# Optimization experiments

Hardware: AMD Instinct MI355X
Metric: run time of the kernel (lower is better)

## Reference

```python
import jax, jax.numpy as jnp
import numpy as np

G = 64        # graphs per batch
NPG = 1024    # nodes per graph (static)
DEG = 8       # avg degree
INF = 128
HID = 256
OUT = 256
N = G * NPG
E = N * DEG
K1 = 512      # ceil(0.5 * 1024)
K2 = 256      # ceil(0.5 * 512)
EPS = 1e-5


def setup_inputs() -> dict:
    key = jax.random.key(0)
    ks = jax.random.split(key, 12)
    s = 0.05
    x = jax.random.normal(ks[0], (N, INF), jnp.float32)
    off = (jnp.arange(G, dtype=jnp.int32) * NPG)[:, None]
    src = (jax.random.randint(ks[1], (G, NPG * DEG), 0, NPG, jnp.int32) + off).reshape(-1)
    dst = (jax.random.randint(ks[2], (G, NPG * DEG), 0, NPG, jnp.int32) + off).reshape(-1)
    return {
        'x': x, 'src': src, 'dst': dst,
        'W_rel1': jax.random.normal(ks[3], (INF, HID), jnp.float32) * s,
        'b_rel1': jnp.zeros((HID,), jnp.float32),
        'W_root1': jax.random.normal(ks[4], (INF, HID), jnp.float32) * s,
        'g1': jnp.ones((HID,), jnp.float32), 'bt1': jnp.zeros((HID,), jnp.float32),
        'p1': jax.random.normal(ks[5], (HID,), jnp.float32) * s,
        'g2': jnp.ones((HID,), jnp.float32), 'bt2': jnp.zeros((HID,), jnp.float32),
        'W_rel2': jax.random.normal(ks[6], (HID, HID), jnp.float32) * s,
        'b_rel2': jnp.zeros((HID,), jnp.float32),
        'W_root2': jax.random.normal(ks[7], (HID, HID), jnp.float32) * s,
        'p2': jax.random.normal(ks[8], (HID,), jnp.float32) * s,
        'Wl': jax.random.normal(ks[9], (2 * HID, OUT), jnp.float32) * s,
        'bl': jnp.zeros((OUT,), jnp.float32),
    }


def _bn(x, g, b):
    # training-mode BatchNorm over nodes (biased variance), as nn.BatchNorm1d
    m = x.mean(0)
    v = x.var(0)
    return (x - m) * jax.lax.rsqrt(v + EPS) * g + b


def _conv(x, src, dst, emask, W_rel, b_rel, W_root):
    # GraphConv: sum_{j->i} x_j, then lin_rel(aggr) + lin_root(x)
    msg = x[src]                                    # [E, F] gather
    if emask is not None:
        msg = jnp.where(emask[:, None], msg, 0.0)   # dropped edges contribute 0
    agg = jax.ops.segment_sum(msg, dst, num_segments=x.shape[0])
    return agg @ W_rel + b_rel + x @ W_root


def _pool(x, src, dst, emask, p, n, k):
    # TopKPooling: score = tanh((x.p)/||p||); keep top-k per graph; x *= score
    score = jnp.tanh((x @ p) / jnp.linalg.norm(p))  # [G*n]
    vals, idx = jax.lax.top_k(score.reshape(G, n), k)   # [G, k] per-graph
    perm = (idx + (jnp.arange(G, dtype=jnp.int32) * n)[:, None]).reshape(-1)
    xn = x[perm] * vals.reshape(-1)[:, None]        # [G*k, F]
    # remap old node ids -> new ids; -1 marks dropped nodes
    mapping = jnp.full((G * n,), -1, jnp.int32).at[perm].set(
        jnp.arange(G * k, dtype=jnp.int32))
    ns, nd = mapping[src], mapping[dst]
    nmask = emask & (ns >= 0) & (nd >= 0)
    ns = jnp.where(nmask, ns, 0)
    nd = jnp.where(nmask, nd, 0)
    return xn, ns, nd, nmask


def reference(x, src, dst, W_rel1, b_rel1, W_root1, g1, bt1, p1,
              g2, bt2, W_rel2, b_rel2, W_root2, p2, Wl, bl):
    act = lambda v: jax.nn.gelu(v, approximate=False)
    h = _conv(x, src, dst, None, W_rel1, b_rel1, W_root1)
    h = _bn(act(h), g1, bt1)
    h, s1, d1, m1 = _pool(h, src, dst, jnp.ones((E,), bool), p1, NPG, K1)
    hg = h.reshape(G, K1, HID)
    x1 = jnp.concatenate([hg.max(1), hg.mean(1)], axis=1)   # [G, 2H] gmp|gap
    h = act(_bn(h, g2, bt2))
    h = _conv(h, s1, d1, m1, W_rel2, b_rel2, W_root2)
    h, s2, d2, m2 = _pool(h, s1, d1, m1, p2, K1, K2)
    hg = h.reshape(G, K2, HID)
    x2 = jnp.concatenate([hg.max(1), hg.mean(1)], axis=1)
    return (x1 + x2) @ Wl + bl                              # [G, OUT]
```

## Files before the change

### kernel.cpp

```cpp
#include <hip/hip_runtime.h>
#include <hip/hip_bf16.h>
#include <float.h>

#define GG    64
#define NPG   1024
#define EPG   8192
#define NE    524288
#define FIN   128
#define HID   256
#define K1    512
#define K2    256
#define NN0   65536
#define NN1   32768
#define NN2   16384
#define EPSBN 1e-5f

typedef _Float16 f16x8 __attribute__((ext_vector_type(8)));
typedef _Float16 f16x4 __attribute__((ext_vector_type(4)));
typedef float f32x4 __attribute__((ext_vector_type(4)));

__device__ __forceinline__ float gelu_exact(float v) {
    return 0.5f * v * (1.0f + erff(v * 0.7071067811865476f));
}

__device__ __forceinline__ void gld16(const void* g, void* lds) {
    __builtin_amdgcn_global_load_lds(
        (const __attribute__((address_space(1))) unsigned int*)g,
        (__attribute__((address_space(3))) unsigned int*)lds, 16, 0, 0);
}

__global__ __launch_bounds__(512) void k_prepcsr(
        const int* __restrict__ src, const int* __restrict__ dst,
        int* __restrict__ rowp, int* __restrict__ ssrc, int* __restrict__ map1,
        const float* __restrict__ Wrel1, const float* __restrict__ Wroot1,
        const float* __restrict__ Wrel2, const float* __restrict__ Wroot2,
        const float* __restrict__ p2,
        _Float16* __restrict__ W1h, _Float16* __restrict__ W2h,
        float* __restrict__ q2, float* __restrict__ stats1,
        float* __restrict__ stats2) {
    __shared__ int cnt[NPG];
    __shared__ int sa[NPG];
    __shared__ int sb[NPG];
    __shared__ float red[256];
    const int b = blockIdx.x, tid = threadIdx.x;
    if (b < 64) {
        const int g = b;
        const int eb = g * EPG;
        for (int i = g * 512 + tid; i < NN0; i += GG * 512) map1[i] = -1;
        for (int i = tid; i < NPG; i += 512) cnt[i] = 0;
        __syncthreads();
        for (int e = tid; e < EPG; e += 512)
            atomicAdd(&cnt[dst[eb + e] & (NPG - 1)], 1);
        __syncthreads();
        for (int i = tid; i < NPG; i += 512) sa[i] = cnt[i];
        __syncthreads();
        int* cur = sa; int* nxt = sb;
        for (int d = 1; d < NPG; d <<= 1) {
            for (int i = tid; i < NPG; i += 512)
                nxt[i] = cur[i] + ((i >= d) ? cur[i - d] : 0);
            __syncthreads();
            int* t = cur; cur = nxt; nxt = t;
        }
        for (int i = tid; i < NPG; i += 512) {
            const int st = cur[i] - cnt[i];
            rowp[g * (NPG + 1) + i] = st;
            cnt[i] = st;
        }
        if (tid == 0) rowp[g * (NPG + 1) + NPG] = EPG;
        __syncthreads();
        for (int e = tid; e < EPG; e += 512) {
            const int d = dst[eb + e] & (NPG - 1);
            const int p = atomicAdd(&cnt[d], 1);
            ssrc[eb + p] = src[eb + e] & (NPG - 1);
        }
    } else if (b < 192) {
        const int i = (b - 64) * 512 + tid;
        const int n = i >> 8, k = i & 255;
        const float v = (k < FIN) ? Wrel1[k * HID + n] : Wroot1[(k - FIN) * HID + n];
        W1h[i] = (_Float16)v;
    } else if (b < 448) {
        const int i = (b - 192) * 512 + tid;
        const int n = i >> 9, k = i & 511;
        const float v = (k < HID) ? Wrel2[k * HID + n] : Wroot2[(k - HID) * HID + n];
        W2h[i] = (_Float16)v;
    } else if (b == 448) {
        if (tid < 256) { const float pv = p2[tid]; red[tid] = pv * pv; }
        __syncthreads();
        for (int s = 128; s > 0; s >>= 1) {
            if (tid < s) red[tid] += red[tid + s];
            __syncthreads();
        }
        if (tid < 256) q2[tid] = p2[tid] * rsqrtf(red[0]);
    } else {
        stats1[tid] = 0.f;
        stats2[tid] = 0.f;
    }
}

__global__ __launch_bounds__(256) void k_agg1(const float* __restrict__ x,
        const int* __restrict__ rowp, const int* __restrict__ ssrc,
        _Float16* __restrict__ A1) {
    const int b = blockIdx.x;
    const int g = b & 63;
    const int ng = b >> 6;
    const int tid = threadIdx.x;
    const int ln = tid & 31;
    const int node = (ng << 3) + (tid >> 5);
    const int s0 = rowp[g * (NPG + 1) + node];
    const int s1 = rowp[g * (NPG + 1) + node + 1];
    const float4* x4 = reinterpret_cast<const float4*>(x);
    const size_t gb = (size_t)(g << 10) * 32;
    const int* sp = ssrc + (size_t)g * EPG;
    float4 acc = make_float4(0.f, 0.f, 0.f, 0.f);
    for (int j = s0; j < s1; ++j) {
        const float4 v = x4[gb + (size_t)sp[j] * 32 + ln];
        acc.x += v.x; acc.y += v.y; acc.z += v.z; acc.w += v.w;
    }
    const size_t rb = ((size_t)((g << 10) + node)) * 256;
    *reinterpret_cast<f16x4*>(&A1[rb + (ln << 2)]) =
        (f16x4){(_Float16)acc.x, (_Float16)acc.y, (_Float16)acc.z, (_Float16)acc.w};
    const float4 xv = x4[gb + (size_t)node * 32 + ln];
    *reinterpret_cast<f16x4*>(&A1[rb + 128 + (ln << 2)]) =
        (f16x4){(_Float16)xv.x, (_Float16)xv.y, (_Float16)xv.z, (_Float16)xv.w};
}

__global__ __launch_bounds__(256) void k_agg2(const _Float16* __restrict__ A2r,
        const int* __restrict__ rowp, const int* __restrict__ ssrc,
        const int* __restrict__ perm1, const int* __restrict__ map1,
        _Float16* __restrict__ A2w) {
    const int b = blockIdx.x;
    const int g = b & 63;
    const int ng = b >> 6;
    const int tid = threadIdx.x;
    const int ln = tid & 63;
    const int ni = (ng << 2) + (tid >> 6);
    const int on = perm1[(g << 9) + ni] & (NPG - 1);
    const int s0 = rowp[g * (NPG + 1) + on];
    const int s1 = rowp[g * (NPG + 1) + on + 1];
    const int* sp = ssrc + (size_t)g * EPG;
    const int* mp = map1 + ((size_t)g << 10);
    float4 acc = make_float4(0.f, 0.f, 0.f, 0.f);
    for (int j = s0; j < s1; ++j) {
        const int ms = mp[sp[j]];
        if (ms < 0) continue;
        const f16x4 v = *reinterpret_cast<const f16x4*>(
            &A2r[(size_t)ms * 512 + 256 + (ln << 2)]);
        acc.x += (float)v[0]; acc.y += (float)v[1];
        acc.z += (float)v[2]; acc.w += (float)v[3];
    }
    *reinterpret_cast<f16x4*>(&A2w[((size_t)((g << 9) + ni)) * 512 + (ln << 2)]) =
        (f16x4){(_Float16)acc.x, (_Float16)acc.y, (_Float16)acc.z, (_Float16)acc.w};
}

template<int K, int EPI, int MCH>
__global__ __launch_bounds__(512, 2) void k_gemmB(
        const _Float16* __restrict__ A, const _Float16* __restrict__ B,
        const float* __restrict__ bias, _Float16* __restrict__ C,
        float* __restrict__ stats, const float* __restrict__ qv2,
        float* __restrict__ scores, int M) {
    __shared__ _Float16 Bs[256 * 256];
    __shared__ float csum[256];
    __shared__ float csq[256];
    const int tid = threadIdx.x;
    const int l = tid & 63, w = tid >> 6;
    constexpr int BM = 8 * MCH * 16;
    const int m0 = blockIdx.x * BM;
    const int r16 = l & 15, kg = l >> 4;

    f32x4 acc[MCH][16] = {};
    constexpr int PH = K / 256;

#pragma unroll
    for (int ph = 0; ph < PH; ++ph) {
        if (ph) __syncthreads();
        for (int u = tid; u < 8192; u += 512) {
            const int row = u >> 5, slot = u & 31;
            const int gch = slot ^ (row & 7);
            gld16(B + (size_t)row * K + ph * 256 + gch * 8, (char*)Bs + u * 16);
        }
        asm volatile("s_waitcnt vmcnt(0)" ::: "memory");
        __syncthreads();

#pragma unroll
        for (int ks = 0; ks < 8; ++ks) {
            f16x8 a[MCH];
#pragma unroll
            for (int mc = 0; mc < MCH; ++mc) {
                const int mrow = m0 + (w * MCH + mc) * 16 + r16;
                a[mc] = *reinterpret_cast<const f16x8*>(
                    A + (size_t)mrow * K + ph * 256 + ks * 32 + kg * 8);
            }
#pragma unroll
            for (int ni = 0; ni < 16; ++ni) {
                const int brow = ni * 16 + r16;
                const int c = ks * 4 + kg;
                const int pos = c ^ (brow & 7);
                const f16x8 bf = *reinterpret_cast<const f16x8*>(
                    (const char*)Bs + (brow * 32 + pos) * 16);
#pragma unroll
                for (int mc = 0; mc < MCH; ++mc)
                    acc[mc][ni] = __builtin_amdgcn_mfma_f32_16x16x32_f16(
                        a[mc], bf, acc[mc][ni], 0, 0, 0);
            }
        }
    }

    if (EPI == 1) {
        __syncthreads();
        if (tid < 256) { csum[tid] = 0.f; csq[tid] = 0.f; }
        __syncthreads();
    }

    float sp[MCH][4];
    if (EPI == 2) {
#pragma unroll
        for (int mc = 0; mc < MCH; ++mc)
#pragma unroll
            for (int r = 0; r < 4; ++r) sp[mc][r] = 0.f;
    }
#pragma unroll
    for (int ni = 0; ni < 16; ++ni) {
        const int col = ni * 16 + r16;
        const float bc = bias[col];
        const float qvn = (EPI == 2) ? qv2[col] : 0.f;
        float sA = 0.f, qA = 0.f;
#pragma unroll
        for (int mc = 0; mc < MCH; ++mc) {
#pragma unroll
            for (int r = 0; r < 4; ++r) {
                const int row = m0 + (w * MCH + mc) * 16 + (kg << 2) + r;
                float t = acc[mc][ni][r] + bc;
                if (EPI == 1) {
                    t = gelu_exact(t);
                    sA += t;
                    qA += t * t;
                }
                if (EPI == 2) sp[mc][r] += t * qvn;
                C[(size_t)row * 256 + col] = (_Float16)t;
            }
        }
        if (EPI == 1) {
            unsafeAtomicAdd(&csum[col], sA);
            unsafeAtomicAdd(&csq[col], qA);
        }
    }
    if (EPI == 1) {
        __syncthreads();
        if (tid < 256) {
            unsafeAtomicAdd(&stats[tid], csum[tid]);
            unsafeAtomicAdd(&stats[HID + tid], csq[tid]);
        }
    }
    if (EPI == 2) {
#pragma unroll
        for (int mc = 0; mc < MCH; ++mc)
#pragma unroll
            for (int r = 0; r < 4; ++r) {
                float s = sp[mc][r];
                s += __shfl_xor(s, 1);
                s += __shfl_xor(s, 2);
                s += __shfl_xor(s, 4);
                s += __shfl_xor(s, 8);
                if (r16 == 0)
                    scores[m0 + (w * MCH + mc) * 16 + (kg << 2) + r] = s;
            }
    }
}

__global__ __launch_bounds__(256) void k_finalize1(const float* __restrict__ stats,
        const float* __restrict__ g1, const float* __restrict__ bt1,
        const float* __restrict__ p1, float* __restrict__ scale,
        float* __restrict__ shift, float* __restrict__ q, float* __restrict__ r) {
    __shared__ float red[256];
    const int c = threadIdx.x;
    const float m = stats[c] * (1.f / NN0);
    const float v = stats[HID + c] * (1.f / NN0) - m * m;
    const float sc = g1[c] * rsqrtf(v + EPSBN);
    const float sh = bt1[c] - m * sc;
    scale[c] = sc;
    shift[c] = sh;
    const float pv = p1[c];
    red[c] = pv * pv;
    __syncthreads();
    for (int s = 128; s > 0; s >>= 1) {
        if (c < s) red[c] += red[c + s];
        __syncthreads();
    }
    const float inv = rsqrtf(red[0]);
    q[c] = sc * pv * inv;
    __syncthreads();
    red[c] = sh * pv * inv;
    __syncthreads();
    for (int s = 128; s > 0; s >>= 1) {
        if (c < s) red[c] += red[c + s];
        __syncthreads();
    }
    if (c == 0) r[0] = red[0];
}

__global__ __launch_bounds__(256) void k_finalize2(const float* __restrict__ stats,
        const float* __restrict__ g2, const float* __restrict__ bt2,
        float* __restrict__ scale, float* __restrict__ shift) {
    const int c = threadIdx.x;
    const float m = stats[c] * (1.f / NN1);
    const float v = stats[HID + c] * (1.f / NN1) - m * m;
    const float sc = g2[c] * rsqrtf(v + EPSBN);
    scale[c] = sc;
    shift[c] = bt2[c] - m * sc;
}

__global__ __launch_bounds__(256) void k_score(const _Float16* __restrict__ H,
        const float* __restrict__ q, const float* __restrict__ r,
        float* __restrict__ out) {
    const int node = blockIdx.x * 4 + (threadIdx.x >> 6);
    const int lane = threadIdx.x & 63;
    const f16x4 h = *reinterpret_cast<const f16x4*>(H + (size_t)node * HID + (lane << 2));
    const float4 qv = *reinterpret_cast<const float4*>(q + (lane << 2));
    float d = (float)h[0] * qv.x + (float)h[1] * qv.y +
              (float)h[2] * qv.z + (float)h[3] * qv.w;
#pragma unroll
    for (int off = 32; off > 0; off >>= 1) d += __shfl_xor(d, off);
    if (lane == 0) out[node] = d + (r ? r[0] : 0.f);
}

template<int NN_, int KK_, int NT_>
__global__ __launch_bounds__(NT_) void k_topk(const float* __restrict__ scores,
        int nparts, int pstride, int* __restrict__ perm,
        float* __restrict__ vals, int* __restrict__ mapping) {
    __shared__ float s[NN_];
    __shared__ int id[NN_];
    const int g = blockIdx.x, tid = threadIdx.x;
    for (int i = tid; i < NN_; i += NT_) {
        float raw = 0.f;
        for (int p = 0; p < nparts; ++p)
            raw += scores[(size_t)p * pstride + g * NN_ + i];
        s[i] = tanhf(raw);
        id[i] = i;
    }
    __syncthreads();
    for (int k = 2; k <= NN_; k <<= 1) {
        for (int j = k >> 1; j > 0; j >>= 1) {
            for (int t = tid; t < NN_; t += NT_) {
                const int ixj = t ^ j;
                if (ixj > t) {
                    const bool desc = ((t & k) == 0);
                    const float s1 = s[t], s2 = s[ixj];
                    const int i1 = id[t], i2 = id[ixj];
                    const bool inOrder = (s1 > s2) || (s1 == s2 && i1 < i2);
                    if (inOrder != desc) { s[t] = s2; s[ixj] = s1; id[t] = i2; id[ixj] = i1; }
                }
            }
            __syncthreads();
        }
    }
    for (int i = tid; i < KK_; i += NT_) {
        const int oid = id[i];
        perm[g * KK_ + i] = g * NN_ + oid;
        vals[g * KK_ + i] = s[i];
        if (mapping) mapping[g * NN_ + oid] = g * KK_ + i;
    }
}

__global__ __launch_bounds__(256) void k_pool1p(const _Float16* __restrict__ HG,
        const int* __restrict__ perm, const float* __restrict__ vals,
        const float* __restrict__ scale1, const float* __restrict__ shift1,
        float* __restrict__ pmax, float* __restrict__ psum,
        float* __restrict__ psq) {
    const int b = blockIdx.x;
    const int g = b >> 3, ig = b & 7;
    const int c = threadIdx.x;
    const float sc = scale1[c], sh = shift1[c];
    float mx = -FLT_MAX, sm = 0.f, sq = 0.f;
    for (int i = ig * 64; i < ig * 64 + 64; ++i) {
        const int idx = (g << 9) + i;
        const int srow = perm[idx];
        const float val = vals[idx];
        const float hv = (float)HG[(size_t)srow * HID + c];
        const float xn = (hv * sc + sh) * val;
        mx = fmaxf(mx, xn);
        sm += xn;
        sq += xn * xn;
    }
    pmax[b * 256 + c] = mx;
    psum[b * 256 + c] = sm;
    psq[b * 256 + c] = sq;
}

__global__ __launch_bounds__(256) void k_pool1r(const float* __restrict__ pmax,
        const float* __restrict__ psum, const float* __restrict__ psq,
        float* __restrict__ X1, float* __restrict__ stats2) {
    const int g = blockIdx.x, c = threadIdx.x;
    float mx = -FLT_MAX, sm = 0.f, sq = 0.f;
    for (int ig = 0; ig < 8; ++ig) {
        const int o = ((g << 3) + ig) * 256 + c;
        mx = fmaxf(mx, pmax[o]);
        sm += psum[o];
        sq += psq[o];
    }
    X1[g * 512 + c] = mx;
    X1[g * 512 + 256 + c] = sm * (1.f / K1);
    unsafeAtomicAdd(&stats2[c], sm);
    unsafeAtomicAdd(&stats2[HID + c], sq);
}

__global__ __launch_bounds__(256) void k_h2in(const _Float16* __restrict__ HG,
        const int* __restrict__ perm, const float* __restrict__ vals,
        const float* __restrict__ scale1, const float* __restrict__ shift1,
        const float* __restrict__ scale2, const float* __restrict__ shift2,
        _Float16* __restrict__ A2) {
    const int i = blockIdx.x * 256 + threadIdx.x;
    const int idx = i >> 6, c4 = i & 63;
    const int srow = perm[idx];
    const float val = vals[idx];
    const f16x4 h = *reinterpret_cast<const f16x4*>(&HG[(size_t)srow * HID + (c4 << 2)]);
    const float4 s1 = reinterpret_cast<const float4*>(scale1)[c4];
    const float4 b1 = reinterpret_cast<const float4*>(shift1)[c4];
    const float4 s2 = reinterpret_cast<const float4*>(scale2)[c4];
    const float4 b2 = reinterpret_cast<const float4*>(shift2)[c4];
    const float x0 = ((float)h[0] * s1.x + b1.x) * val;
    const float x1 = ((float)h[1] * s1.y + b1.y) * val;
    const float x2 = ((float)h[2] * s1.z + b1.z) * val;
    const float x3 = ((float)h[3] * s1.w + b1.w) * val;
    *reinterpret_cast<f16x4*>(&A2[(size_t)idx * 512 + 256 + (c4 << 2)]) =
        (f16x4){(_Float16)gelu_exact(x0 * s2.x + b2.x),
                (_Float16)gelu_exact(x1 * s2.y + b2.y),
                (_Float16)gelu_exact(x2 * s2.z + b2.z),
                (_Float16)gelu_exact(x3 * s2.w + b2.w)};
}

__global__ __launch_bounds__(256) void k_x2p(const _Float16* __restrict__ H2,
        const int* __restrict__ perm, const float* __restrict__ vals,
        float* __restrict__ pmax, float* __restrict__ psum) {
    const int b = blockIdx.x;
    const int g = b >> 3, ig = b & 7;
    const int c = threadIdx.x;
    float mx = -FLT_MAX, sm = 0.f;
    for (int i = ig * 32; i < ig * 32 + 32; ++i) {
        const int idx = (g << 8) + i;
        const int srow = perm[idx];
        const float v = (float)H2[(size_t)srow * HID + c] * vals[idx];
        mx = fmaxf(mx, v);
        sm += v;
    }
    pmax[b * 256 + c] = mx;
    psum[b * 256 + c] = sm;
}

__global__ __launch_bounds__(256) void k_x2final(const float* __restrict__ pmax,
        const float* __restrict__ psum, const float* __restrict__ X1,
        const float* __restrict__ Wl, const float* __restrict__ bl,
        float* __restrict__ out) {
    __shared__ float sx2[512];
    const int g = blockIdx.x, c = threadIdx.x;
    float mx = -FLT_MAX, sm = 0.f;
    for (int ig = 0; ig < 8; ++ig) {
        const int o = ((g << 3) + ig) * 256 + c;
        mx = fmaxf(mx, pmax[o]);
        sm += psum[o];
    }
    sx2[c] = mx;
    sx2[256 + c] = sm * (1.f / K2);
    __syncthreads();
    float acc = bl[c];
    for (int k = 0; k < 512; ++k) {
        const float xv = X1[g * 512 + k] + sx2[k];
        acc = fmaf(xv, Wl[k * HID + c], acc);
    }
    out[g * HID + c] = acc;
}

extern "C" void kernel_launch(void* const* d_in, const int* in_sizes, int n_in,
                              void* d_out, int out_size, void* d_ws, size_t ws_size,
                              hipStream_t stream) {
    (void)in_sizes; (void)n_in; (void)out_size; (void)ws_size;
    const float* x       = (const float*)d_in[0];
    const int*   src     = (const int*)  d_in[1];
    const int*   dst     = (const int*)  d_in[2];
    const float* W_rel1  = (const float*)d_in[3];
    const float* b_rel1  = (const float*)d_in[4];
    const float* W_root1 = (const float*)d_in[5];
    const float* g1      = (const float*)d_in[6];
    const float* bt1     = (const float*)d_in[7];
    const float* p1      = (const float*)d_in[8];
    const float* g2      = (const float*)d_in[9];
    const float* bt2     = (const float*)d_in[10];
    const float* W_rel2  = (const float*)d_in[11];
    const float* b_rel2  = (const float*)d_in[12];
    const float* W_root2 = (const float*)d_in[13];
    const float* p2      = (const float*)d_in[14];
    const float* Wl      = (const float*)d_in[15];
    const float* bl      = (const float*)d_in[16];
    float* out = (float*)d_out;

    char* w = (char*)d_ws;
    size_t off = 0;
    auto alloc = [&](size_t bytes) -> void* {
        void* p = w + off;
        off += (bytes + 255) & ~(size_t)255;
        return p;
    };
    _Float16* A1  = (_Float16*)alloc((size_t)NN0 * 256 * 2);
    _Float16* HG  = (_Float16*)alloc((size_t)NN0 * 256 * 2);
    _Float16* H2  = (_Float16*)alloc((size_t)NN1 * 256 * 2);
    int*   ROWP   = (int*)  alloc((size_t)GG * (NPG + 1) * 4);
    int*   SSRC   = (int*)  alloc((size_t)NE * 4);
    float* SCORES = (float*)alloc((size_t)NN0 * 4);
    int*   PERM1  = (int*)  alloc((size_t)NN1 * 4);
    float* VALS1  = (float*)alloc((size_t)NN1 * 4);
    int*   MAP1   = (int*)  alloc((size_t)NN0 * 4);
    int*   PERM2  = (int*)  alloc((size_t)NN2 * 4);
    float* VALS2  = (float*)alloc((size_t)NN2 * 4);
    float* STATS1 = (float*)alloc(512 * 4);
    float* STATS2 = (float*)alloc(512 * 4);
    float* SCALE1 = (float*)alloc(256 * 4);
    float* SHIFT1 = (float*)alloc(256 * 4);
    float* Q1     = (float*)alloc(256 * 4);
    float* R1     = (float*)alloc(256);
    float* SCALE2 = (float*)alloc(256 * 4);
    float* SHIFT2 = (float*)alloc(256 * 4);
    float* Q2     = (float*)alloc(256 * 4);
    _Float16* W1h = (_Float16*)alloc((size_t)256 * 256 * 2);
    _Float16* W2h = (_Float16*)alloc((size_t)256 * 512 * 2);
    float* X1     = (float*)alloc((size_t)GG * 512 * 4);
    float* PMAX   = (float*)alloc((size_t)512 * 256 * 4);
    float* PSUM   = (float*)alloc((size_t)512 * 256 * 4);
    float* PSQ    = (float*)alloc((size_t)512 * 256 * 4);
    _Float16* A2 = A1;

    k_prepcsr<<<450, 512, 0, stream>>>(src, dst, ROWP, SSRC, MAP1,
        W_rel1, W_root1, W_rel2, W_root2, p2, W1h, W2h, Q2, STATS1, STATS2);
    k_agg1<<<8192, 256, 0, stream>>>(x, ROWP, SSRC, A1);
    k_gemmB<256, 1, 2><<<256, 512, 0, stream>>>(A1, W1h, b_rel1, HG, STATS1,
        nullptr, nullptr, NN0);
    k_finalize1<<<1, 256, 0, stream>>>(STATS1, g1, bt1, p1, SCALE1, SHIFT1, Q1, R1);
    k_score<<<NN0 / 4, 256, 0, stream>>>(HG, Q1, R1, SCORES);
    k_topk<NPG, K1, 512><<<GG, 512, 0, stream>>>(SCORES, 1, 0, PERM1, VALS1, MAP1);
    k_pool1p<<<512, 256, 0, stream>>>(HG, PERM1, VALS1, SCALE1, SHIFT1, PMAX, PSUM, PSQ);
    k_pool1r<<<GG, 256, 0, stream>>>(PMAX, PSUM, PSQ, X1, STATS2);
    k_finalize2<<<1, 256, 0, stream>>>(STATS2, g2, bt2, SCALE2, SHIFT2);
    k_h2in<<<8192, 256, 0, stream>>>(HG, PERM1, VALS1, SCALE1, SHIFT1,
        SCALE2, SHIFT2, A2);
    k_agg2<<<8192, 256, 0, stream>>>(A2, ROWP, SSRC, PERM1, MAP1, A2);
    k_gemmB<512, 2, 1><<<256, 512, 0, stream>>>(A2, W2h, b_rel2, H2, nullptr,
        Q2, SCORES, NN1);
    k_topk<K1, K2, 256><<<GG, 256, 0, stream>>>(SCORES, 1, 0, PERM2, VALS2, nullptr);
    k_x2p<<<512, 256, 0, stream>>>(H2, PERM2, VALS2, PMAX, PSUM);
    k_x2final<<<GG, 256, 0, stream>>>(PMAX, PSUM, X1, Wl, bl, out);
}
```

Baseline: 253.0 us.

## Retile GEMM into 256x128 output blocks split across a 2D grid

```diff
diff --git a/kernel.cpp b/kernel.cpp
--- a/kernel.cpp
+++ b/kernel.cpp
@@ -152,53 +152,53 @@
         (f16x4){(_Float16)acc.x, (_Float16)acc.y, (_Float16)acc.z, (_Float16)acc.w};
 }
 
-template<int K, int EPI, int MCH>
+template<int K, int EPI>
 __global__ __launch_bounds__(512, 2) void k_gemmB(
         const _Float16* __restrict__ A, const _Float16* __restrict__ B,
         const float* __restrict__ bias, _Float16* __restrict__ C,
         float* __restrict__ stats, const float* __restrict__ qv2,
         float* __restrict__ scores, int M) {
-    __shared__ _Float16 Bs[256 * 256];
-    __shared__ float csum[256];
-    __shared__ float csq[256];
+    __shared__ _Float16 Bs[128 * 256];
+    __shared__ float csum[128];
+    __shared__ float csq[128];
     const int tid = threadIdx.x;
     const int l = tid & 63, w = tid >> 6;
-    constexpr int BM = 8 * MCH * 16;
-    const int m0 = blockIdx.x * BM;
+    const int wr = w >> 1, wc = w & 1;
+    const int m0 = blockIdx.x * 256, n0 = blockIdx.y * 128;
     const int r16 = l & 15, kg = l >> 4;
 
-    f32x4 acc[MCH][16] = {};
+    f32x4 acc[4][4] = {};
     constexpr int PH = K / 256;
 
 #pragma unroll
     for (int ph = 0; ph < PH; ++ph) {
         if (ph) __syncthreads();
-        for (int u = tid; u < 8192; u += 512) {
+        for (int u = tid; u < 4096; u += 512) {
             const int row = u >> 5, slot = u & 31;
             const int gch = slot ^ (row & 7);
-            gld16(B + (size_t)row * K + ph * 256 + gch * 8, (char*)Bs + u * 16);
+            gld16(B + (size_t)(n0 + row) * K + ph * 256 + gch * 8,
+                  (char*)Bs + u * 16);
         }
         asm volatile("s_waitcnt vmcnt(0)" ::: "memory");
         __syncthreads();
 
 #pragma unroll
         for (int ks = 0; ks < 8; ++ks) {
-            f16x8 a[MCH];
-#pragma unroll
-            for (int mc = 0; mc < MCH; ++mc) {
-                const int mrow = m0 + (w * MCH + mc) * 16 + r16;
+            f16x8 a[4];
+#pragma unroll
+            for (int mc = 0; mc < 4; ++mc) {
+                const int mrow = m0 + wr * 64 + mc * 16 + r16;
                 a[mc] = *reinterpret_cast<const f16x8*>(
                     A + (size_t)mrow * K + ph * 256 + ks * 32 + kg * 8);
             }
 #pragma unroll
-            for (int ni = 0; ni < 16; ++ni) {
-                const int brow = ni * 16 + r16;
-                const int c = ks * 4 + kg;
-                const int pos = c ^ (brow & 7);
+            for (int ni = 0; ni < 4; ++ni) {
+                const int brow = wc * 64 + ni * 16 + r16;
+                const int pos = (ks * 4 + kg) ^ (brow & 7);
                 const f16x8 bf = *reinterpret_cast<const f16x8*>(
                     (const char*)Bs + (brow * 32 + pos) * 16);
 #pragma unroll
-                for (int mc = 0; mc < MCH; ++mc)
+                for (int mc = 0; mc < 4; ++mc)
                     acc[mc][ni] = __builtin_amdgcn_mfma_f32_16x16x32_f16(
                         a[mc], bf, acc[mc][ni], 0, 0, 0);
             }
@@ -207,53 +207,55 @@
 
     if (EPI == 1) {
         __syncthreads();
-        if (tid < 256) { csum[tid] = 0.f; csq[tid] = 0.f; }
-        __syncthreads();
-    }
-
-    float sp[MCH][4];
+        if (tid < 128) { csum[tid] = 0.f; csq[tid] = 0.f; }
+        __syncthreads();
+    }
+
+    float qv[4];
     if (EPI == 2) {
 #pragma unroll
-        for (int mc = 0; mc < MCH; ++mc)
-#pragma unroll
-            for (int r = 0; r < 4; ++r) sp[mc][r] = 0.f;
-    }
-#pragma unroll
-    for (int ni = 0; ni < 16; ++ni) {
-        const int col = ni * 16 + r16;
-        const float bc = bias[col];
-        const float qvn = (EPI == 2) ? qv2[col] : 0.f;
-        float sA = 0.f, qA = 0.f;
-#pragma unroll
-        for (int mc = 0; mc < MCH; ++mc) {
+        for (int ni = 0; ni < 4; ++ni)
+            qv[ni] = qv2[n0 + wc * 64 + ni * 16 + r16];
+    }
+    float sA[4] = {0, 0, 0, 0};
+    float qA[4] = {0, 0, 0, 0};
+    float sp[4][4] = {};
+#pragma unroll
+    for (int mc = 0; mc < 4; ++mc)
+#pragma unroll
+        for (int ni = 0; ni < 4; ++ni) {
+            const int cl = wc * 64 + ni * 16 + r16;
+            const float bc = bias[n0 + cl];
 #pragma unroll
             for (int r = 0; r < 4; ++r) {
-                const int row = m0 + (w * MCH + mc) * 16 + (kg << 2) + r;
+                const int row = m0 + wr * 64 + mc * 16 + (kg << 2) + r;
                 float t = acc[mc][ni][r] + bc;
                 if (EPI == 1) {
                     t = gelu_exact(t);
-                    sA += t;
-                    qA += t * t;
+                    sA[ni] += t;
+                    qA[ni] += t * t;
                 }
-                if (EPI == 2) sp[mc][r] += t * qvn;
-                C[(size_t)row * 256 + col] = (_Float16)t;
+                if (EPI == 2) sp[mc][r] += t * qv[ni];
+                C[(size_t)row * 256 + n0 + cl] = (_Float16)t;
             }
         }
-        if (EPI == 1) {
-            unsafeAtomicAdd(&csum[col], sA);
-            unsafeAtomicAdd(&csq[col], qA);
-        }
-    }
     if (EPI == 1) {
-        __syncthreads();
-        if (tid < 256) {
-            unsafeAtomicAdd(&stats[tid], csum[tid]);
-            unsafeAtomicAdd(&stats[HID + tid], csq[tid]);
+#pragma unroll
+        for (int ni = 0; ni < 4; ++ni) {
+            const int cl = wc * 64 + ni * 16 + r16;
+            unsafeAtomicAdd(&csum[cl], sA[ni]);
+            unsafeAtomicAdd(&csq[cl], qA[ni]);
+        }
+        __syncthreads();
+        if (tid < 128) {
+            unsafeAtomicAdd(&stats[n0 + tid], csum[tid]);
+            unsafeAtomicAdd(&stats[HID + n0 + tid], csq[tid]);
         }
     }
     if (EPI == 2) {
-#pragma unroll
-        for (int mc = 0; mc < MCH; ++mc)
+        const int slot = (int)blockIdx.y * 2 + wc;
+#pragma unroll
+        for (int mc = 0; mc < 4; ++mc)
 #pragma unroll
             for (int r = 0; r < 4; ++r) {
                 float s = sp[mc][r];
@@ -262,7 +264,7 @@
                 s += __shfl_xor(s, 4);
                 s += __shfl_xor(s, 8);
                 if (r16 == 0)
-                    scores[m0 + (w * MCH + mc) * 16 + (kg << 2) + r] = s;
+                    scores[(size_t)slot * M + m0 + wr * 64 + mc * 16 + (kg << 2) + r] = s;
             }
     }
 }
@@ -504,7 +506,7 @@
     _Float16* H2  = (_Float16*)alloc((size_t)NN1 * 256 * 2);
     int*   ROWP   = (int*)  alloc((size_t)GG * (NPG + 1) * 4);
     int*   SSRC   = (int*)  alloc((size_t)NE * 4);
-    float* SCORES = (float*)alloc((size_t)NN0 * 4);
+    float* SCORES = (float*)alloc((size_t)4 * NN1 * 4);
     int*   PERM1  = (int*)  alloc((size_t)NN1 * 4);
     float* VALS1  = (float*)alloc((size_t)NN1 * 4);
     int*   MAP1   = (int*)  alloc((size_t)NN0 * 4);
@@ -530,7 +532,7 @@
     k_prepcsr<<<450, 512, 0, stream>>>(src, dst, ROWP, SSRC, MAP1,
         W_rel1, W_root1, W_rel2, W_root2, p2, W1h, W2h, Q2, STATS1, STATS2);
     k_agg1<<<8192, 256, 0, stream>>>(x, ROWP, SSRC, A1);
-    k_gemmB<256, 1, 2><<<256, 512, 0, stream>>>(A1, W1h, b_rel1, HG, STATS1,
+    k_gemmB<256, 1><<<dim3(256, 2), 512, 0, stream>>>(A1, W1h, b_rel1, HG, STATS1,
         nullptr, nullptr, NN0);
     k_finalize1<<<1, 256, 0, stream>>>(STATS1, g1, bt1, p1, SCALE1, SHIFT1, Q1, R1);
     k_score<<<NN0 / 4, 256, 0, stream>>>(HG, Q1, R1, SCORES);
@@ -541,9 +543,9 @@
     k_h2in<<<8192, 256, 0, stream>>>(HG, PERM1, VALS1, SCALE1, SHIFT1,
         SCALE2, SHIFT2, A2);
     k_agg2<<<8192, 256, 0, stream>>>(A2, ROWP, SSRC, PERM1, MAP1, A2);
-    k_gemmB<512, 2, 1><<<256, 512, 0, stream>>>(A2, W2h, b_rel2, H2, nullptr,
+    k_gemmB<512, 2><<<dim3(128, 2), 512, 0, stream>>>(A2, W2h, b_rel2, H2, nullptr,
         Q2, SCORES, NN1);
-    k_topk<K1, K2, 256><<<GG, 256, 0, stream>>>(SCORES, 1, 0, PERM2, VALS2, nullptr);
+    k_topk<K1, K2, 256><<<GG, 256, 0, stream>>>(SCORES, 4, NN1, PERM2, VALS2, nullptr);
     k_x2p<<<512, 256, 0, stream>>>(H2, PERM2, VALS2, PMAX, PSUM);
     k_x2final<<<GG, 256, 0, stream>>>(PMAX, PSUM, X1, Wl, bl, out);
 }
```

New measurement: 277.9 us. 9.8% more time.
